# Kernel tuning notes

Measured on AMD Instinct MI355X. Metric: run time of the kernel, lower is better.

Reference implementation:

```python
import jax, jax.numpy as jnp
import numpy as np

B, S, D, H, BLK = 2, 2048, 1024, 16, 128
DH = D // H
NB = S // BLK
EPS = 1e-5
NEG = -1e9


def _make_layout():
    i = np.arange(NB)[:, None]
    j = np.arange(NB)[None, :]
    # causal: local block diagonal + previous block + global first block column
    lay = ((j == i) | (j == i - 1) | (j == 0)) & (j <= i)
    return jnp.asarray(np.broadcast_to(lay, (H, NB, NB)).astype(np.int32))


def setup_inputs() -> dict:
    key = jax.random.key(0)
    ks = jax.random.split(key, 8)
    sd = 1.0 / np.sqrt(D)
    inp = {
        "x": jax.random.normal(ks[0], (B, S, D), jnp.float32),
        "ln1_g": jnp.ones((D,), jnp.float32),
        "ln1_b": jnp.zeros((D,), jnp.float32),
        "Wq": jax.random.normal(ks[1], (D, D), jnp.float32) * sd,
        "bq": jnp.zeros((D,), jnp.float32),
        "Wk": jax.random.normal(ks[2], (D, D), jnp.float32) * sd,
        "bk": jnp.zeros((D,), jnp.float32),
        "Wv": jax.random.normal(ks[3], (D, D), jnp.float32) * sd,
        "bv": jnp.zeros((D,), jnp.float32),
        "Wo": jax.random.normal(ks[4], (D, D), jnp.float32) * sd,
        "bo": jnp.zeros((D,), jnp.float32),
        "ln2_g": jnp.ones((D,), jnp.float32),
        "ln2_b": jnp.zeros((D,), jnp.float32),
        "W1": jax.random.normal(ks[5], (D, 4 * D), jnp.float32) * sd,
        "b1": jnp.zeros((4 * D,), jnp.float32),
        "W2": jax.random.normal(ks[6], (4 * D, D), jnp.float32) * (1.0 / np.sqrt(4 * D)),
        "b2": jnp.zeros((D,), jnp.float32),
        "layout": _make_layout(),
    }
    return inp


def _ln(x, g, b):
    m = jnp.mean(x, -1, keepdims=True)
    v = jnp.var(x, -1, keepdims=True)
    return (x - m) * jax.lax.rsqrt(v + EPS) * g + b


def reference(x, ln1_g, ln1_b, Wq, bq, Wk, bk, Wv, bv, Wo, bo,
              ln2_g, ln2_b, W1, b1, W2, b2, layout):
    # ---- pre-norm block-sparse multi-head attention + residual ----
    h = _ln(x, ln1_g, ln1_b)
    q = (h @ Wq + bq).reshape(B, S, H, DH).transpose(0, 2, 1, 3)
    k = (h @ Wk + bk).reshape(B, S, H, DH).transpose(0, 2, 1, 3)
    v = (h @ Wv + bv).reshape(B, S, H, DH).transpose(0, 2, 1, 3)

    # expand block layout [H,NB,NB] -> token mask [H,S,S], intersect with causal
    blk_mask = jnp.repeat(jnp.repeat(layout > 0, BLK, axis=1), BLK, axis=2)
    causal = jnp.tril(jnp.ones((S, S), bool))
    mask = blk_mask & causal  # [H,S,S]

    scale = DH ** -0.5
    scores = jnp.einsum("bhqd,bhkd->bhqk", q * scale, k)
    scores = jnp.where(mask[None], scores, NEG)
    att = jax.nn.softmax(scores, axis=-1)
    ctx = jnp.einsum("bhqk,bhkd->bhqd", att, v)
    ctx = ctx.transpose(0, 2, 1, 3).reshape(B, S, D)
    x = x + (ctx @ Wo + bo)

    # ---- pre-norm MLP (GeLU) + residual ----
    h2 = _ln(x, ln2_g, ln2_b)
    ff = jax.nn.gelu(h2 @ W1 + b1, approximate=False) @ W2 + b2
    return x + ff
```

## Files before the change

kernel.cpp:

```cpp
#include <hip/hip_runtime.h>

typedef unsigned short ushort;
typedef unsigned int uint;
typedef __attribute__((ext_vector_type(8))) short short8;
typedef __attribute__((ext_vector_type(4))) float floatx4;

#define DEV __device__ __forceinline__

DEV ushort f2bf(float f) {
    uint u = __float_as_uint(f);
    u += 0x7fffu + ((u >> 16) & 1u);
    return (ushort)(u >> 16);
}

DEV void load_lds16(const void* g, const void* l) {
    __builtin_amdgcn_global_load_lds(
        (const __attribute__((address_space(1))) void*)g,
        (__attribute__((address_space(3))) void*)l, 16, 0, 0);
}

template<int ROWS>
DEV void stage_tile(const ushort* g, int ldg, ushort* lds, int w, int lane) {
#pragma unroll
    for (int t = 0; t < ROWS / 32; ++t) {
        int row = t * 32 + w * 8 + (lane >> 3);
        int cg  = (lane & 7) ^ (row & 7);
        load_lds16(g + (size_t)row * ldg + cg * 8, lds + (t * 32 + w * 8) * 64);
    }
}

DEV short8 frag_ld(const ushort* lds, int row, int ks, int quad) {
    int slot = (ks * 4 + quad) ^ (row & 7);
    return *(const short8*)(lds + row * 64 + slot * 8);
}

__global__ __launch_bounds__(256) void prep_kernel(
    const float* __restrict__ Wq, const float* __restrict__ Wk,
    const float* __restrict__ Wv, const float* __restrict__ Wo,
    const float* __restrict__ W1, const float* __restrict__ W2,
    const float* __restrict__ bq, const float* __restrict__ bk,
    const float* __restrict__ bv,
    ushort* __restrict__ wqkvT, ushort* __restrict__ woT,
    ushort* __restrict__ w1T, ushort* __restrict__ w2T,
    float* __restrict__ bqkv,
    const float* __restrict__ x, const float* __restrict__ ln1g,
    const float* __restrict__ ln1b, ushort* __restrict__ hb) {
    __shared__ float t[64][65];
    int bid = blockIdx.x;
    int tid = threadIdx.x;
    if (bid >= 3072) {
        int row = bid - 3072;
        float4 v = ((const float4*)(x + (size_t)row * 1024))[tid];
        float s = v.x + v.y + v.z + v.w;
        float q = v.x * v.x + v.y * v.y + v.z * v.z + v.w * v.w;
#pragma unroll
        for (int m = 1; m < 64; m <<= 1) {
            s += __shfl_xor(s, m);
            q += __shfl_xor(q, m);
        }
        float* ss = &t[0][0];
        float* qs = &t[1][0];
        int w = tid >> 6;
        if ((tid & 63) == 0) { ss[w] = s; qs[w] = q; }
        __syncthreads();
        s = ss[0] + ss[1] + ss[2] + ss[3];
        q = qs[0] + qs[1] + qs[2] + qs[3];
        float mean = s * (1.0f / 1024.0f);
        float var  = q * (1.0f / 1024.0f) - mean * mean;
        float rs   = rsqrtf(var + 1e-5f);
        float4 gv = ((const float4*)ln1g)[tid];
        float4 bv4 = ((const float4*)ln1b)[tid];
        uint lo = f2bf((v.x - mean) * rs * gv.x + bv4.x) |
                  ((uint)f2bf((v.y - mean) * rs * gv.y + bv4.y) << 16);
        uint hi = f2bf((v.z - mean) * rs * gv.z + bv4.z) |
                  ((uint)f2bf((v.w - mean) * rs * gv.w + bv4.w) << 16);
        ((uint2*)(hb + (size_t)row * 1024))[tid] = make_uint2(lo, hi);
        return;
    }
    const float* in; ushort* out; int K, N, tx, ty;
    if (bid < 1024) {
        int m = bid >> 8, r = bid & 255;
        in  = m == 0 ? Wq : (m == 1 ? Wk : (m == 2 ? Wv : Wo));
        out = m < 3 ? wqkvT + (size_t)m * 1024 * 1024 : woT;
        K = 1024; N = 1024; tx = r & 15; ty = r >> 4;
    } else if (bid < 2048) {
        int r = bid - 1024; in = W1; out = w1T; K = 1024; N = 4096; tx = r & 63; ty = r >> 6;
    } else {
        int r = bid - 2048; in = W2; out = w2T; K = 4096; N = 1024; tx = r & 15; ty = r >> 4;
    }
    int txx = tid & 63, tyy = tid >> 6;
    int k0 = ty * 64, n0 = tx * 64;
#pragma unroll
    for (int r2 = tyy; r2 < 64; r2 += 4)
        t[r2][txx] = in[(size_t)(k0 + r2) * N + n0 + txx];
    __syncthreads();
#pragma unroll
    for (int r2 = tyy; r2 < 64; r2 += 4)
        out[(size_t)(n0 + r2) * K + k0 + txx] = f2bf(t[txx][r2]);
    if (bid < 12) {
        int i = bid * 256 + tid;
        bqkv[i] = i < 1024 ? bq[i] : (i < 2048 ? bk[i - 1024] : bv[i - 2048]);
    }
}

__global__ __launch_bounds__(256) void ln_kernel(const float* __restrict__ x,
                                                 const float* __restrict__ g,
                                                 const float* __restrict__ bb,
                                                 ushort* __restrict__ out) {
    int row = blockIdx.x, tid = threadIdx.x;
    float4 v = ((const float4*)(x + (size_t)row * 1024))[tid];
    float s = v.x + v.y + v.z + v.w;
    float q = v.x * v.x + v.y * v.y + v.z * v.z + v.w * v.w;
#pragma unroll
    for (int m = 1; m < 64; m <<= 1) {
        s += __shfl_xor(s, m);
        q += __shfl_xor(q, m);
    }
    __shared__ float ss[4], qs[4];
    int w = tid >> 6;
    if ((tid & 63) == 0) { ss[w] = s; qs[w] = q; }
    __syncthreads();
    s = ss[0] + ss[1] + ss[2] + ss[3];
    q = qs[0] + qs[1] + qs[2] + qs[3];
    float mean = s * (1.0f / 1024.0f);
    float var  = q * (1.0f / 1024.0f) - mean * mean;
    float rs   = rsqrtf(var + 1e-5f);
    float4 gv = ((const float4*)g)[tid];
    float4 bv = ((const float4*)bb)[tid];
    uint lo = f2bf((v.x - mean) * rs * gv.x + bv.x) |
              ((uint)f2bf((v.y - mean) * rs * gv.y + bv.y) << 16);
    uint hi = f2bf((v.z - mean) * rs * gv.z + bv.z) |
              ((uint)f2bf((v.w - mean) * rs * gv.w + bv.w) << 16);
    ((uint2*)(out + (size_t)row * 1024))[tid] = make_uint2(lo, hi);
}

__global__ __launch_bounds__(256) void combine2(const float* __restrict__ p,
                                                const float* __restrict__ res,
                                                const float* __restrict__ bias,
                                                float* __restrict__ out,
                                                int MN, int N) {
    int idx = (blockIdx.x * 256 + threadIdx.x) * 4;
    float4 a = *(const float4*)(p + idx);
    float4 b = *(const float4*)(p + MN + idx);
    float4 r = *(const float4*)(res + idx);
    float4 bi = *(const float4*)(bias + (idx & (N - 1)));
    float4 o;
    o.x = a.x + b.x + r.x + bi.x;
    o.y = a.y + b.y + r.y + bi.y;
    o.z = a.z + b.z + r.z + bi.z;
    o.w = a.w + b.w + r.w + bi.w;
    *(float4*)(out + idx) = o;
}

template<int MODE>
__global__ __launch_bounds__(256, 2) void gemm_db(const ushort* __restrict__ A,
                                                  const ushort* __restrict__ Bt,
                                                  const float* __restrict__ bias,
                                                  const float* __restrict__ res,
                                                  void* __restrict__ outp,
                                                  int M, int N, int K, int ksplit,
                                                  int stx_n, int per_xcd) {
    constexpr int BUFE = 256 * 64;
    __shared__ ushort smem[2 * BUFE];
    int tid = threadIdx.x, w = tid >> 6, lane = tid & 63;
    int quad = lane >> 4, l15 = lane & 15;
    int wm = w >> 1, wn = w & 1;

    int flat = blockIdx.x;
    int xcd = flat & 7, slot = flat >> 3;
    int st = xcd * per_xcd + (slot >> 4);
    int li = slot & 15;
    int bx = (st % stx_n) * 4 + (li & 3);
    int by = (st / stx_n) * 4 + (li >> 2);
    int m0 = by * 128, n0 = bx * 128;
    int sk = blockIdx.y, KS = K / ksplit;
    int kbeg = sk * KS, kend = kbeg + KS;

    const ushort* Ab = A + (size_t)m0 * K;
    const ushort* Bb = Bt + (size_t)n0 * K;

    stage_tile<128>(Ab + kbeg, K, smem, w, lane);
    stage_tile<128>(Bb + kbeg, K, smem + 128 * 64, w, lane);

    floatx4 acc[4][4] = {};
    int cur = 0;
    for (int k0 = kbeg; k0 < kend; k0 += 64) {
        __syncthreads();
        if (k0 + 64 < kend) {
            ushort* nb = smem + (cur ^ 1) * BUFE;
            stage_tile<128>(Ab + k0 + 64, K, nb, w, lane);
            stage_tile<128>(Bb + k0 + 64, K, nb + 128 * 64, w, lane);
        }
        const ushort* Asc = smem + cur * BUFE;
        const ushort* Bsc = Asc + 128 * 64;
#pragma unroll
        for (int ks = 0; ks < 2; ++ks) {
            short8 af[4], bfr[4];
#pragma unroll
            for (int i = 0; i < 4; ++i) af[i] = frag_ld(Asc, wm * 64 + i * 16 + l15, ks, quad);
#pragma unroll
            for (int j = 0; j < 4; ++j) bfr[j] = frag_ld(Bsc, wn * 64 + j * 16 + l15, ks, quad);
#pragma unroll
            for (int i = 0; i < 4; ++i)
#pragma unroll
                for (int j = 0; j < 4; ++j)
                    acc[i][j] = __builtin_amdgcn_mfma_f32_16x16x32_bf16(bfr[j], af[i], acc[i][j], 0, 0, 0);
        }
        cur ^= 1;
    }

    ushort* Sb = smem;
    float*  Sf = (float*)smem;
    int rl  = wm * 16 + l15;
    int rl2 = tid >> 3, c8 = tid & 7;
    if (MODE <= 1) {
#pragma unroll
        for (int i = 0; i < 4; ++i) {
            __syncthreads();
#pragma unroll
            for (int j = 0; j < 4; ++j) {
                int col = wn * 64 + j * 16 + quad * 4;
                float4 bv4 = *(const float4*)(bias + n0 + col);
                float v0 = acc[i][j][0] + bv4.x, v1 = acc[i][j][1] + bv4.y;
                float v2 = acc[i][j][2] + bv4.z, v3 = acc[i][j][3] + bv4.w;
                if (MODE == 1) {
                    v0 = 0.5f * v0 * (1.0f + erff(v0 * 0.70710678118f));
                    v1 = 0.5f * v1 * (1.0f + erff(v1 * 0.70710678118f));
                    v2 = 0.5f * v2 * (1.0f + erff(v2 * 0.70710678118f));
                    v3 = 0.5f * v3 * (1.0f + erff(v3 * 0.70710678118f));
                }
                uint lo = f2bf(v0) | ((uint)f2bf(v1) << 16);
                uint hi = f2bf(v2) | ((uint)f2bf(v3) << 16);
                *(uint2*)(Sb + rl * 136 + col) = make_uint2(lo, hi);
            }
            __syncthreads();
            int grow = m0 + (rl2 >> 4) * 64 + i * 16 + (rl2 & 15);
            short8 d0 = *(short8*)(Sb + rl2 * 136 + c8 * 8);
            short8 d1 = *(short8*)(Sb + rl2 * 136 + 64 + c8 * 8);
            if (MODE == 1) {
                ushort* op = (ushort*)outp + (size_t)grow * N + n0 + c8 * 8;
                *(short8*)op = d0;
                *(short8*)(op + 64) = d1;
            } else {
                int b = grow >> 11, s = grow & 2047;
                int which = n0 >> 10, nbase = n0 & 1023;
                int h0 = nbase >> 6;
                size_t a0 = (size_t)which * 4194304 +
                            (((size_t)(b * 16 + h0)) * 2048 + s) * 64 + c8 * 8;
                size_t a1 = (size_t)which * 4194304 +
                            (((size_t)(b * 16 + h0 + 1)) * 2048 + s) * 64 + c8 * 8;
                *(short8*)((ushort*)outp + a0) = d0;
                *(short8*)((ushort*)outp + a1) = d1;
            }
        }
    } else {
#pragma unroll
        for (int i = 0; i < 4; ++i) {
#pragma unroll
            for (int hh = 0; hh < 2; ++hh) {
                __syncthreads();
                if (wn == hh) {
#pragma unroll
                    for (int j = 0; j < 4; ++j) {
                        float4 wv;
                        wv.x = acc[i][j][0]; wv.y = acc[i][j][1];
                        wv.z = acc[i][j][2]; wv.w = acc[i][j][3];
                        *(float4*)(Sf + rl * 68 + j * 16 + quad * 4) = wv;
                    }
                }
                __syncthreads();
                int grow = m0 + (rl2 >> 4) * 64 + i * 16 + (rl2 & 15);
                int gc = n0 + hh * 64 + c8 * 8;
                float4 u0 = *(float4*)(Sf + rl2 * 68 + c8 * 8);
                float4 u1 = *(float4*)(Sf + rl2 * 68 + c8 * 8 + 4);
                if (MODE == 3) {
                    float* op = (float*)outp + (size_t)sk * M * N + (size_t)grow * N + gc;
                    *(float4*)op = u0;
                    *(float4*)(op + 4) = u1;
                } else {
                    float4 b0 = *(const float4*)(bias + gc);
                    float4 b1 = *(const float4*)(bias + gc + 4);
                    const float* rp = res + (size_t)grow * N + gc;
                    float4 r0 = *(const float4*)rp;
                    float4 r1 = *(const float4*)(rp + 4);
                    float4 o0, o1;
                    o0.x = u0.x + b0.x + r0.x; o0.y = u0.y + b0.y + r0.y;
                    o0.z = u0.z + b0.z + r0.z; o0.w = u0.w + b0.w + r0.w;
                    o1.x = u1.x + b1.x + r1.x; o1.y = u1.y + b1.y + r1.y;
                    o1.z = u1.z + b1.z + r1.z; o1.w = u1.w + b1.w + r1.w;
                    float* op = (float*)outp + (size_t)grow * N + gc;
                    *(float4*)op = o0;
                    *(float4*)(op + 4) = o1;
                }
            }
        }
    }
}

__global__ __launch_bounds__(256) void attn_kernel(const ushort* __restrict__ qg,
                                                   const ushort* __restrict__ kg,
                                                   const ushort* __restrict__ vg,
                                                   ushort* __restrict__ ctx) {
    __shared__ ushort Qs[64 * 64];
    __shared__ ushort Ks[128 * 64];
    __shared__ ushort Vs[64 * 136];
    __shared__ ushort Ps[64 * 136];
    int iq2 = blockIdx.x, h = blockIdx.y, b = blockIdx.z;
    int tid = threadIdx.x, w = tid >> 6, lane = tid & 63;
    int quad = lane >> 4, l15 = lane & 15;
    int iq = iq2 >> 1;

    const ushort* qp    = qg + ((size_t)(b * 16 + h) * 2048 + iq2 * 64) * 64;
    const ushort* kbase = kg + (size_t)(b * 16 + h) * 2048 * 64;
    const ushort* vbase = vg + (size_t)(b * 16 + h) * 2048 * 64;

    stage_tile<64>(qp, 64, Qs, w, lane);

    floatx4 o[4] = {};
    float mi[4], li[4];
#pragma unroll
    for (int r = 0; r < 4; ++r) { mi[r] = -1e30f; li[r] = 0.0f; }

    int jbs[3];
    int nj = 0;
    jbs[nj++] = 0;
    if (iq > 1) jbs[nj++] = iq - 1;
    if (iq > 0) jbs[nj++] = iq;

    for (int ji = 0; ji < nj; ++ji) {
        int jb = jbs[ji];
        __syncthreads();
        stage_tile<128>(kbase + (size_t)jb * 128 * 64, 64, Ks, w, lane);
        {
            int dh = tid & 63, sg = tid >> 6;
            const ushort* vp = vbase + (size_t)jb * 128 * 64;
#pragma unroll
            for (int cc = 0; cc < 8; ++cc) {
                int s0 = sg * 32 + cc * 4;
                ushort e0 = vp[(s0 + 0) * 64 + dh];
                ushort e1 = vp[(s0 + 1) * 64 + dh];
                ushort e2 = vp[(s0 + 2) * 64 + dh];
                ushort e3 = vp[(s0 + 3) * 64 + dh];
                uint lo = e0 | ((uint)e1 << 16), hi = e2 | ((uint)e3 << 16);
                *(uint2*)(Vs + dh * 136 + s0) = make_uint2(lo, hi);
            }
        }
        __syncthreads();

        floatx4 sacc[8] = {};
#pragma unroll
        for (int ks = 0; ks < 2; ++ks) {
            short8 af = frag_ld(Qs, w * 16 + l15, ks, quad);
            short8 bf8[8];
#pragma unroll
            for (int nt = 0; nt < 8; ++nt) bf8[nt] = frag_ld(Ks, nt * 16 + l15, ks, quad);
#pragma unroll
            for (int nt = 0; nt < 8; ++nt)
                sacc[nt] = __builtin_amdgcn_mfma_f32_16x16x32_bf16(af, bf8[nt], sacc[nt], 0, 0, 0);
        }

        float rowmax[4] = {-1e30f, -1e30f, -1e30f, -1e30f};
        bool diag = (jb == iq);
        int rowL0 = (iq2 & 1) * 64 + w * 16 + quad * 4;
#pragma unroll
        for (int nt = 0; nt < 8; ++nt) {
#pragma unroll
            for (int r = 0; r < 4; ++r) {
                float xv = sacc[nt][r] * 0.125f;
                if (diag && (nt * 16 + l15 > rowL0 + r)) xv = -1e30f;
                sacc[nt][r] = xv;
                rowmax[r] = fmaxf(rowmax[r], xv);
            }
        }
#pragma unroll
        for (int r = 0; r < 4; ++r)
#pragma unroll
            for (int m = 1; m < 16; m <<= 1)
                rowmax[r] = fmaxf(rowmax[r], __shfl_xor(rowmax[r], m));

        float alpha[4], rsum[4];
#pragma unroll
        for (int r = 0; r < 4; ++r) {
            float mnew = fmaxf(mi[r], rowmax[r]);
            alpha[r] = __expf(mi[r] - mnew);
            mi[r] = mnew;
            rsum[r] = 0.0f;
        }
#pragma unroll
        for (int nt = 0; nt < 8; ++nt) {
#pragma unroll
            for (int r = 0; r < 4; ++r) {
                float p = __expf(sacc[nt][r] - mi[r]);
                rsum[r] += p;
                Ps[(w * 16 + quad * 4 + r) * 136 + nt * 16 + l15] = f2bf(p);
            }
        }
#pragma unroll
        for (int r = 0; r < 4; ++r) {
#pragma unroll
            for (int m = 1; m < 16; m <<= 1) rsum[r] += __shfl_xor(rsum[r], m);
            li[r] = li[r] * alpha[r] + rsum[r];
        }
#pragma unroll
        for (int nt = 0; nt < 4; ++nt)
#pragma unroll
            for (int r = 0; r < 4; ++r) o[nt][r] *= alpha[r];

#pragma unroll
        for (int ks2 = 0; ks2 < 4; ++ks2) {
            short8 ap = *(const short8*)(Ps + (w * 16 + l15) * 136 + ks2 * 32 + quad * 8);
            short8 bv4[4];
#pragma unroll
            for (int nt = 0; nt < 4; ++nt)
                bv4[nt] = *(const short8*)(Vs + (nt * 16 + l15) * 136 + ks2 * 32 + quad * 8);
#pragma unroll
            for (int nt = 0; nt < 4; ++nt)
                o[nt] = __builtin_amdgcn_mfma_f32_16x16x32_bf16(ap, bv4[nt], o[nt], 0, 0, 0);
        }
    }
#pragma unroll
    for (int nt = 0; nt < 4; ++nt) {
#pragma unroll
        for (int r = 0; r < 4; ++r) {
            int srow = iq2 * 64 + w * 16 + quad * 4 + r;
            float val = o[nt][r] / li[r];
            ctx[((size_t)b * 2048 + srow) * 1024 + h * 64 + nt * 16 + l15] = f2bf(val);
        }
    }
}

extern "C" void kernel_launch(void* const* d_in, const int* in_sizes, int n_in,
                              void* d_out, int out_size, void* d_ws, size_t ws_size,
                              hipStream_t stream) {
    (void)in_sizes; (void)n_in; (void)out_size; (void)ws_size;
    const float* x    = (const float*)d_in[0];
    const float* ln1g = (const float*)d_in[1];
    const float* ln1b = (const float*)d_in[2];
    const float* Wq   = (const float*)d_in[3];
    const float* bq   = (const float*)d_in[4];
    const float* Wk   = (const float*)d_in[5];
    const float* bk   = (const float*)d_in[6];
    const float* Wv   = (const float*)d_in[7];
    const float* bv   = (const float*)d_in[8];
    const float* Wo   = (const float*)d_in[9];
    const float* bo   = (const float*)d_in[10];
    const float* ln2g = (const float*)d_in[11];
    const float* ln2b = (const float*)d_in[12];
    const float* W1   = (const float*)d_in[13];
    const float* b1   = (const float*)d_in[14];
    const float* W2   = (const float*)d_in[15];
    const float* b2   = (const float*)d_in[16];

    char* ws = (char*)d_ws;
    size_t off = 0;
    auto alloc = [&](size_t bytes) {
        char* p = ws + off;
        off += (bytes + 255) & ~(size_t)255;
        return p;
    };
    ushort* wqkvT = (ushort*)alloc((size_t)3072 * 1024 * 2);
    ushort* woT   = (ushort*)alloc((size_t)1024 * 1024 * 2);
    ushort* w1T   = (ushort*)alloc((size_t)1024 * 4096 * 2);
    ushort* w2T   = (ushort*)alloc((size_t)4096 * 1024 * 2);
    float*  bqkv  = (float*)alloc((size_t)3072 * 4);
    ushort* hb    = (ushort*)alloc((size_t)4096 * 1024 * 2);
    ushort* qkvb  = (ushort*)alloc((size_t)3 * 4096 * 1024 * 2);
    ushort* ctx   = (ushort*)alloc((size_t)4096 * 1024 * 2);
    float*  x1    = (float*)alloc((size_t)4096 * 1024 * 4);
    ushort* h2    = (ushort*)alloc((size_t)4096 * 1024 * 2);
    ushort* ub    = (ushort*)alloc((size_t)4096 * 4096 * 2);
    float* w2p = (float*)hb;

    prep_kernel<<<7168, 256, 0, stream>>>(Wq, Wk, Wv, Wo, W1, W2, bq, bk, bv,
                                          wqkvT, woT, w1T, w2T, bqkv,
                                          x, ln1g, ln1b, hb);

    gemm_db<0><<<dim3(768, 1), 256, 0, stream>>>(hb, wqkvT, bqkv, nullptr, qkvb,
                                                 4096, 3072, 1024, 1, 6, 6);

    attn_kernel<<<dim3(32, 16, 2), 256, 0, stream>>>(qkvb, qkvb + 4194304,
                                                     qkvb + 2 * 4194304, ctx);

    gemm_db<2><<<dim3(256, 1), 256, 0, stream>>>(ctx, woT, bo, x, x1,
                                                 4096, 1024, 1024, 1, 2, 2);

    ln_kernel<<<4096, 256, 0, stream>>>(x1, ln2g, ln2b, h2);

    gemm_db<1><<<dim3(1024, 1), 256, 0, stream>>>(h2, w1T, b1, nullptr, ub,
                                                  4096, 4096, 1024, 1, 8, 8);

    gemm_db<3><<<dim3(256, 2), 256, 0, stream>>>(ub, w2T, b2, nullptr, w2p,
                                                 4096, 1024, 4096, 2, 2, 2);
    combine2<<<4096, 256, 0, stream>>>(w2p, x1, b2, (float*)d_out,
                                       4096 * 1024, 1024);
}
```

Baseline: 323.6 us.

## Add 256x256-tile 8-wave GEMM with interleaved staging for QKV and MLP GEMMs

Adds a new GEMM kernel with 256x256 output tiles computed by 512 threads (8 waves). It streams half-tiles into double-buffered LDS between MFMA quadrants, using raw barriers, explicit waitcnt and setprio to overlap loads with math. The QKV, W1 and W2 GEMMs now use it. W2 changes from a 2-way to a 4-way split-K, with a 4-input combine kernel and one partial buffer aliased onto the start of the workspace. The larger tiles aim to raise data reuse and MFMA utilisation, but the hand-written sync and workspace aliasing risk races, and the extra split-K partials add memory traffic.

```diff
diff --git a/kernel.cpp b/kernel.cpp
--- a/kernel.cpp
+++ b/kernel.cpp
@@ -29,9 +29,54 @@
     }
 }
 
+DEV void stage_half(const ushort* g, int ldg, ushort* lds, int w, int lane) {
+#pragma unroll
+    for (int t = 0; t < 2; ++t) {
+        int row = t * 64 + w * 8 + (lane >> 3);
+        int cg  = (lane & 7) ^ (row & 7);
+        load_lds16(g + (size_t)row * ldg + cg * 8, lds + (t * 64 + w * 8) * 64);
+    }
+}
+
 DEV short8 frag_ld(const ushort* lds, int row, int ks, int quad) {
     int slot = (ks * 4 + quad) ^ (row & 7);
     return *(const short8*)(lds + row * 64 + slot * 8);
+}
+
+DEV void barrier_raw() { __builtin_amdgcn_s_barrier(); asm volatile("" ::: "memory"); }
+DEV void wait_vm4()   { asm volatile("s_waitcnt vmcnt(4)" ::: "memory"); }
+DEV void wait_vm0()   { asm volatile("s_waitcnt vmcnt(0)" ::: "memory"); }
+DEV void wait_lgkm0() { asm volatile("s_waitcnt lgkmcnt(0)" ::: "memory"); }
+
+template<int MH>
+DEV void read_a(short8 (&a4)[4][2], const ushort* buf, int wm, int l15, int quad) {
+#pragma unroll
+    for (int q = 0; q < 4; ++q)
+#pragma unroll
+        for (int ks = 0; ks < 2; ++ks)
+            a4[q][ks] = frag_ld(buf, wm * 128 + MH * 64 + q * 16 + l15, ks, quad);
+}
+template<int NH>
+DEV void read_b(short8 (&bs)[2][2], const ushort* buf, int wn, int l15, int quad) {
+#pragma unroll
+    for (int j = 0; j < 2; ++j)
+#pragma unroll
+        for (int ks = 0; ks < 2; ++ks)
+            bs[j][ks] = frag_ld(buf, wn * 64 + NH * 32 + j * 16 + l15, ks, quad);
+}
+template<int MH, int NH>
+DEV void mfma_quad(floatx4 (&acc)[8][4], const short8 (&a4)[4][2],
+                   const short8 (&bs)[2][2]) {
+    __builtin_amdgcn_s_setprio(1);
+#pragma unroll
+    for (int q = 0; q < 4; ++q)
+#pragma unroll
+        for (int j = 0; j < 2; ++j)
+#pragma unroll
+            for (int ks = 0; ks < 2; ++ks)
+                acc[MH * 4 + q][NH * 2 + j] = __builtin_amdgcn_mfma_f32_16x16x32_bf16(
+                    bs[j][ks], a4[q][ks], acc[MH * 4 + q][NH * 2 + j], 0, 0, 0);
+    __builtin_amdgcn_s_setprio(0);
 }
 
 __global__ __launch_bounds__(256) void prep_kernel(
@@ -134,21 +179,24 @@
     ((uint2*)(out + (size_t)row * 1024))[tid] = make_uint2(lo, hi);
 }
 
-__global__ __launch_bounds__(256) void combine2(const float* __restrict__ p,
+__global__ __launch_bounds__(256) void combine4(const float* __restrict__ p,
+                                                const float* __restrict__ p3,
                                                 const float* __restrict__ res,
                                                 const float* __restrict__ bias,
                                                 float* __restrict__ out,
                                                 int MN, int N) {
-    int idx = (blockIdx.x * 256 + threadIdx.x) * 4;
-    float4 a = *(const float4*)(p + idx);
-    float4 b = *(const float4*)(p + MN + idx);
+    size_t idx = ((size_t)blockIdx.x * 256 + threadIdx.x) * 4;
+    float4 a0 = *(const float4*)(p + idx);
+    float4 a1 = *(const float4*)(p + (size_t)MN + idx);
+    float4 a2 = *(const float4*)(p + (size_t)2 * MN + idx);
+    float4 a3 = *(const float4*)(p3 + idx);
     float4 r = *(const float4*)(res + idx);
     float4 bi = *(const float4*)(bias + (idx & (N - 1)));
     float4 o;
-    o.x = a.x + b.x + r.x + bi.x;
-    o.y = a.y + b.y + r.y + bi.y;
-    o.z = a.z + b.z + r.z + bi.z;
-    o.w = a.w + b.w + r.w + bi.w;
+    o.x = ((a0.x + a1.x) + (a2.x + a3.x)) + r.x + bi.x;
+    o.y = ((a0.y + a1.y) + (a2.y + a3.y)) + r.y + bi.y;
+    o.z = ((a0.z + a1.z) + (a2.z + a3.z)) + r.z + bi.z;
+    o.w = ((a0.w + a1.w) + (a2.w + a3.w)) + r.w + bi.w;
     *(float4*)(out + idx) = o;
 }
 
@@ -297,6 +345,159 @@
     }
 }
 
+template<int MODE>
+__global__ __launch_bounds__(512, 2) void gemm8(
+    const ushort* __restrict__ A, const ushort* __restrict__ Bt,
+    const float* __restrict__ bias, void* __restrict__ outp,
+    int M, int N, int ldK, int KS, int tiles, int nby) {
+    __shared__ ushort smem[65536];
+    int tid = threadIdx.x, w = tid >> 6, lane = tid & 63;
+    int quad = lane >> 4, l15 = lane & 15;
+    int wm = w >> 2, wn = w & 3;
+
+    int nwg = gridDim.x, bid = blockIdx.x;
+    int swz = (bid & 7) * (nwg >> 3) + (bid >> 3);
+    int sk = swz / tiles, ti = swz - sk * tiles;
+    int nby2 = nby >> 1;
+    int s2 = ti >> 2, q2 = ti & 3;
+    int by = (s2 % nby2) * 2 + (q2 & 1);
+    int bx = (s2 / nby2) * 2 + (q2 >> 1);
+    int m0 = by * 256, n0 = bx * 256;
+
+    const ushort* Ag = A + (size_t)m0 * ldK + (size_t)sk * KS;
+    const ushort* Bg = Bt + (size_t)n0 * ldK + (size_t)sk * KS;
+    ushort* A0 = smem;
+    ushort* B0 = smem + 16384;
+    ushort* A1 = smem + 32768;
+    ushort* B1 = smem + 49152;
+
+    stage_half(Ag,                         ldK, A0,        w, lane);
+    stage_half(Ag + (size_t)128 * ldK,     ldK, A0 + 8192, w, lane);
+    stage_half(Bg,                         ldK, B0,        w, lane);
+    stage_half(Bg + (size_t)128 * ldK,     ldK, B0 + 8192, w, lane);
+    stage_half(Bg + 64,                    ldK, B1,        w, lane);
+    stage_half(Bg + (size_t)128 * ldK + 64, ldK, B1 + 8192, w, lane);
+    wait_vm4();
+    barrier_raw();
+
+    floatx4 acc[8][4] = {};
+    short8 a4[4][2], b0s[2][2], b1s[2][2];
+    int NI = KS >> 7;
+    for (int i = 0; i < NI; ++i) {
+        bool lastI = (i == NI - 1);
+        int ko = i * 128;
+        read_a<0>(a4, A0, wm, l15, quad);
+        read_b<0>(b0s, B0, wn, l15, quad);
+        stage_half(Ag + ko + 64, ldK, A1, w, lane);
+        barrier_raw(); wait_lgkm0();
+        mfma_quad<0, 0>(acc, a4, b0s);
+        barrier_raw();
+        read_b<1>(b1s, B0, wn, l15, quad);
+        stage_half(Ag + (size_t)128 * ldK + ko + 64, ldK, A1 + 8192, w, lane);
+        barrier_raw(); wait_lgkm0();
+        mfma_quad<0, 1>(acc, a4, b1s);
+        barrier_raw();
+        read_a<1>(a4, A0, wm, l15, quad);
+        if (!lastI) stage_half(Bg + ko + 128, ldK, B0, w, lane);
+        barrier_raw(); wait_lgkm0();
+        mfma_quad<1, 1>(acc, a4, b1s);
+        barrier_raw();
+        if (!lastI) stage_half(Bg + (size_t)128 * ldK + ko + 128, ldK, B0 + 8192, w, lane);
+        barrier_raw(); wait_lgkm0();
+        mfma_quad<1, 0>(acc, a4, b0s);
+        if (lastI) wait_vm0(); else wait_vm4();
+        barrier_raw();
+        read_a<0>(a4, A1, wm, l15, quad);
+        read_b<0>(b0s, B1, wn, l15, quad);
+        if (!lastI) stage_half(Ag + ko + 128, ldK, A0, w, lane);
+        barrier_raw(); wait_lgkm0();
+        mfma_quad<0, 0>(acc, a4, b0s);
+        barrier_raw();
+        read_b<1>(b1s, B1, wn, l15, quad);
+        if (!lastI) stage_half(Ag + (size_t)128 * ldK + ko + 128, ldK, A0 + 8192, w, lane);
+        barrier_raw(); wait_lgkm0();
+        mfma_quad<0, 1>(acc, a4, b1s);
+        barrier_raw();
+        read_a<1>(a4, A1, wm, l15, quad);
+        if (!lastI) stage_half(Bg + ko + 192, ldK, B1, w, lane);
+        barrier_raw(); wait_lgkm0();
+        mfma_quad<1, 1>(acc, a4, b1s);
+        barrier_raw();
+        if (!lastI) stage_half(Bg + (size_t)128 * ldK + ko + 192, ldK, B1 + 8192, w, lane);
+        barrier_raw(); wait_lgkm0();
+        mfma_quad<1, 0>(acc, a4, b0s);
+        if (!lastI) wait_vm4();
+        barrier_raw();
+    }
+
+    int sr = wm * 16 + l15;
+    int rl2 = tid >> 4, c15 = tid & 15;
+    int grb = m0 + (rl2 >> 4) * 128 + (rl2 & 15);
+    if (MODE == 3) {
+        float* Sf = (float*)smem;
+        float* obase = (sk < 3) ? (float*)outp + (size_t)sk * M * N
+                                : (float*)bias;
+#pragma unroll
+        for (int mf = 0; mf < 8; ++mf) {
+            barrier_raw();
+#pragma unroll
+            for (int nf = 0; nf < 4; ++nf)
+                *(floatx4*)(Sf + sr * 260 + wn * 64 + nf * 16 + quad * 4) = acc[mf][nf];
+            wait_lgkm0();
+            barrier_raw();
+            int grow = grb + mf * 16;
+            float* op = obase + (size_t)grow * N + n0;
+#pragma unroll
+            for (int k = 0; k < 4; ++k) {
+                int c4 = c15 + 16 * k;
+                *(float4*)(op + c4 * 4) = *(float4*)(Sf + rl2 * 260 + c4 * 4);
+            }
+        }
+    } else {
+        ushort* Sb = smem;
+#pragma unroll
+        for (int mf = 0; mf < 8; ++mf) {
+            barrier_raw();
+#pragma unroll
+            for (int nf = 0; nf < 4; ++nf) {
+                int col = wn * 64 + nf * 16 + quad * 4;
+                float4 bv4 = *(const float4*)(bias + n0 + col);
+                float v0 = acc[mf][nf][0] + bv4.x;
+                float v1 = acc[mf][nf][1] + bv4.y;
+                float v2 = acc[mf][nf][2] + bv4.z;
+                float v3 = acc[mf][nf][3] + bv4.w;
+                if (MODE == 1) {
+                    v0 = 0.5f * v0 * (1.0f + erff(v0 * 0.70710678118f));
+                    v1 = 0.5f * v1 * (1.0f + erff(v1 * 0.70710678118f));
+                    v2 = 0.5f * v2 * (1.0f + erff(v2 * 0.70710678118f));
+                    v3 = 0.5f * v3 * (1.0f + erff(v3 * 0.70710678118f));
+                }
+                uint lo = f2bf(v0) | ((uint)f2bf(v1) << 16);
+                uint hi = f2bf(v2) | ((uint)f2bf(v3) << 16);
+                *(uint2*)(Sb + sr * 264 + col) = make_uint2(lo, hi);
+            }
+            wait_lgkm0();
+            barrier_raw();
+            int grow = grb + mf * 16;
+#pragma unroll
+            for (int cc = 0; cc < 2; ++cc) {
+                int ch = c15 + cc * 16;
+                short8 d = *(const short8*)(Sb + rl2 * 264 + ch * 8);
+                if (MODE == 1) {
+                    *(short8*)((ushort*)outp + (size_t)grow * N + n0 + ch * 8) = d;
+                } else {
+                    int gc = n0 + ch * 8;
+                    int which = gc >> 10, nb2 = gc & 1023;
+                    int hh = nb2 >> 6, dh = nb2 & 63;
+                    int b = grow >> 11, s = grow & 2047;
+                    *(short8*)((ushort*)outp + (size_t)which * 4194304 +
+                               (((size_t)(b * 16 + hh)) * 2048 + s) * 64 + dh) = d;
+                }
+            }
+        }
+    }
+}
+
 __global__ __launch_bounds__(256) void attn_kernel(const ushort* __restrict__ qg,
                                                    const ushort* __restrict__ kg,
                                                    const ushort* __restrict__ vg,
@@ -466,17 +667,18 @@
     ushort* hb    = (ushort*)alloc((size_t)4096 * 1024 * 2);
     ushort* qkvb  = (ushort*)alloc((size_t)3 * 4096 * 1024 * 2);
     ushort* ctx   = (ushort*)alloc((size_t)4096 * 1024 * 2);
+    ushort* h2    = (ushort*)alloc((size_t)4096 * 1024 * 2);
     float*  x1    = (float*)alloc((size_t)4096 * 1024 * 4);
-    ushort* h2    = (ushort*)alloc((size_t)4096 * 1024 * 2);
     ushort* ub    = (ushort*)alloc((size_t)4096 * 4096 * 2);
-    float* w2p = (float*)hb;
+    float* w2p  = (float*)hb;
+    float* w2p3 = (float*)ws;
 
     prep_kernel<<<7168, 256, 0, stream>>>(Wq, Wk, Wv, Wo, W1, W2, bq, bk, bv,
                                           wqkvT, woT, w1T, w2T, bqkv,
                                           x, ln1g, ln1b, hb);
 
-    gemm_db<0><<<dim3(768, 1), 256, 0, stream>>>(hb, wqkvT, bqkv, nullptr, qkvb,
-                                                 4096, 3072, 1024, 1, 6, 6);
+    gemm8<0><<<dim3(192), 512, 0, stream>>>(hb, wqkvT, bqkv, qkvb,
+                                            4096, 3072, 1024, 1024, 192, 16);
 
     attn_kernel<<<dim3(32, 16, 2), 256, 0, stream>>>(qkvb, qkvb + 4194304,
                                                      qkvb + 2 * 4194304, ctx);
@@ -486,11 +688,11 @@
 
     ln_kernel<<<4096, 256, 0, stream>>>(x1, ln2g, ln2b, h2);
 
-    gemm_db<1><<<dim3(1024, 1), 256, 0, stream>>>(h2, w1T, b1, nullptr, ub,
-                                                  4096, 4096, 1024, 1, 8, 8);
-
-    gemm_db<3><<<dim3(256, 2), 256, 0, stream>>>(ub, w2T, b2, nullptr, w2p,
-                                                 4096, 1024, 4096, 2, 2, 2);
-    combine2<<<4096, 256, 0, stream>>>(w2p, x1, b2, (float*)d_out,
+    gemm8<1><<<dim3(256), 512, 0, stream>>>(h2, w1T, b1, ub,
+                                            4096, 4096, 1024, 1024, 256, 16);
+
+    gemm8<3><<<dim3(256), 512, 0, stream>>>(ub, w2T, w2p3, w2p,
+                                            4096, 1024, 4096, 1024, 64, 16);
+    combine4<<<4096, 256, 0, stream>>>(w2p, w2p3, x1, b2, (float*)d_out,
                                        4096 * 1024, 1024);
 }
```

Measured after the change: 337.5 us. +4.3%, slower.
